# Kernel optimization log

Hardware: AMD Instinct MI355X
Metric: run time of the kernel (lower is better)

## Reference

```python
import jax, jax.numpy as jnp
import numpy as np

HID, NH, NKV, HD, BASE = 1536, 24, 6, 64, 10000.0
G = NH // NKV  # kv groups


def setup_inputs() -> dict:
    key = jax.random.key(0)
    k1, k2, k3, k4, k5 = jax.random.split(key, 5)
    B, S = 2, 2048
    s = 0.02
    return {
        "hidden_states": jax.random.normal(k1, (B, S, HID), jnp.float32),
        "position_ids": jnp.broadcast_to(jnp.arange(S, dtype=jnp.int64)[None, :], (B, S)),
        "Wq": jax.random.normal(k2, (NH * HD, HID), jnp.float32) * s,
        "Wk": jax.random.normal(k3, (NKV * HD, HID), jnp.float32) * s,
        "Wv": jax.random.normal(k4, (NKV * HD, HID), jnp.float32) * s,
        "Wo": jax.random.normal(k5, (HID, NH * HD), jnp.float32) * s,
    }


def _rope_tables(seq_len, dtype):
    inv_freq = 1.0 / (BASE ** (jnp.arange(0, HD, 2, dtype=jnp.float32) / HD))
    t = jnp.arange(seq_len, dtype=jnp.float32)
    freqs = jnp.einsum("i,j->ij", t, inv_freq)          # [S, HD/2]
    emb = jnp.concatenate([freqs, freqs], axis=-1)       # [S, HD]
    return jnp.cos(emb).astype(dtype), jnp.sin(emb).astype(dtype)


def _rotate_half(x):
    x1, x2 = x[..., : HD // 2], x[..., HD // 2:]
    return jnp.concatenate([-x2, x1], axis=-1)


def reference(hidden_states, position_ids, Wq, Wk, Wv, Wo):
    B, S, _ = hidden_states.shape
    q = (hidden_states @ Wq.T).reshape(B, S, NH, HD).transpose(0, 2, 1, 3)   # [B,NH,S,D]
    k = (hidden_states @ Wk.T).reshape(B, S, NKV, HD).transpose(0, 2, 1, 3)  # [B,NKV,S,D]
    v = (hidden_states @ Wv.T).reshape(B, S, NKV, HD).transpose(0, 2, 1, 3)

    cos_t, sin_t = _rope_tables(S, hidden_states.dtype)
    cos = cos_t[position_ids][:, None]  # [B,1,S,D]
    sin = sin_t[position_ids][:, None]
    q = q * cos + _rotate_half(q) * sin
    k = k * cos + _rotate_half(k) * sin

    # GQA attention without materializing repeated K/V: view q as [B,NKV,G,S,D]
    qg = q.reshape(B, NKV, G, S, HD)
    scale = 1.0 / np.sqrt(HD)
    scores = jnp.einsum("bkgsd,bktd->bkgst", qg, k) * scale  # [B,NKV,G,S,S]
    causal = jnp.tril(jnp.ones((S, S), dtype=bool))
    scores = jnp.where(causal, scores, jnp.finfo(scores.dtype).min)
    probs = jax.nn.softmax(scores, axis=-1)
    out = jnp.einsum("bkgst,bktd->bkgsd", probs, v)          # [B,NKV,G,S,D]
    out = out.reshape(B, NH, S, HD).transpose(0, 2, 1, 3).reshape(B, S, NH * HD)
    return out @ Wo.T
```

## Files before the change

### kernel.cpp

```cpp
#include <hip/hip_runtime.h>
#include <hip/hip_bf16.h>

#define HIDN 1536
#define NH   24
#define NKV  6
#define HD   64
#define BB   2
#define SS   2048
#define MTOT (BB*SS)
#define NQKV 2304
#define NCHUNK 80
#define LOG2E 1.4426950408889634f

typedef __bf16 bf16x8 __attribute__((ext_vector_type(8)));
typedef float  f32x4  __attribute__((ext_vector_type(4)));
typedef unsigned short u16x8 __attribute__((ext_vector_type(8)));
typedef unsigned int   u32x2 __attribute__((ext_vector_type(2)));

typedef __attribute__((address_space(1))) const unsigned short as1_ushort;
typedef __attribute__((address_space(3))) unsigned short as3_ushort;

__device__ inline float bf2f(unsigned short u) {
    unsigned v = (unsigned)u << 16; float f; __builtin_memcpy(&f, &v, 4); return f;
}
__device__ inline unsigned short f2bf(float f) {
    unsigned u; __builtin_memcpy(&u, &f, 4);
    u = (u + 0x7FFFu + ((u >> 16) & 1u)) >> 16;
    return (unsigned short)u;
}
__device__ inline unsigned cvt_pk_bf16(float lo, float hi) {
    unsigned r;
    asm("v_cvt_pk_bf16_f32 %0, %1, %2" : "=v"(r) : "v"(lo), "v"(hi));
    return r;
}
__device__ inline float exp2_hw(float x) {
    float r;
    asm("v_exp_f32 %0, %1" : "=v"(r) : "v"(x));
    return r;
}
__device__ inline float rowmax16_dpp(float x) {
    int v, r;
    v = __float_as_int(x);
    r = __builtin_amdgcn_update_dpp(v, v, 0x121, 0xF, 0xF, false);
    x = fmaxf(x, __int_as_float(r));
    v = __float_as_int(x);
    r = __builtin_amdgcn_update_dpp(v, v, 0x122, 0xF, 0xF, false);
    x = fmaxf(x, __int_as_float(r));
    v = __float_as_int(x);
    r = __builtin_amdgcn_update_dpp(v, v, 0x124, 0xF, 0xF, false);
    x = fmaxf(x, __int_as_float(r));
    v = __float_as_int(x);
    r = __builtin_amdgcn_update_dpp(v, v, 0x128, 0xF, 0xF, false);
    x = fmaxf(x, __int_as_float(r));
    return x;
}

__global__ __launch_bounds__(256) void k_prep(const float* __restrict__ h_f,
                                              const float* __restrict__ Wq,
                                              const float* __restrict__ Wk,
                                              const float* __restrict__ Wv,
                                              const float* __restrict__ Wo,
                                              unsigned short* __restrict__ h_bf,
                                              unsigned short* __restrict__ qkv_w,
                                              unsigned short* __restrict__ Wo_bf,
                                              float2* __restrict__ cs) {
    int i = blockIdx.x * 256 + threadIdx.x;
    const int nH = MTOT * HIDN / 4;
    const int nQ = HIDN * HIDN / 4;
    const int nK = NKV * HD * HIDN / 4;
    const int nW = 2 * nQ + 2 * nK;
    if (i < nH + nW) {
        const float* src; unsigned short* dst; int j;
        if (i < nH)                    { src = h_f; dst = h_bf;                        j = i; }
        else if ((i -= nH) < nQ)       { src = Wq;  dst = qkv_w;                       j = i; }
        else if (i < nQ + nK)          { src = Wk;  dst = qkv_w + (size_t)nQ * 4;      j = i - nQ; }
        else if (i < nQ + 2 * nK)      { src = Wv;  dst = qkv_w + (size_t)(nQ + nK) * 4; j = i - nQ - nK; }
        else                           { src = Wo;  dst = Wo_bf;                       j = i - nQ - 2 * nK; }
        float4 v = reinterpret_cast<const float4*>(src)[j];
        ushort4 o;
        o.x = f2bf(v.x); o.y = f2bf(v.y); o.z = f2bf(v.z); o.w = f2bf(v.w);
        reinterpret_cast<ushort4*>(dst)[j] = o;
        return;
    }
    int k = i - (nH + nW);
    if (k < SS * 32) {
        int s = k >> 5, f = k & 31;
        double inv = pow(10000.0, -(double)f / 32.0);
        double ang = (double)s * inv;
        cs[k] = make_float2((float)cos(ang), (float)sin(ang));
    }
}

template <typename OutT>
__global__ __launch_bounds__(256) void gemm_bt(const unsigned short* __restrict__ A,
                                               const unsigned short* __restrict__ Bt,
                                               OutT* __restrict__ C,
                                               int N, int K) {
    __shared__ unsigned short Alds[2][128 * 64];
    __shared__ unsigned short Blds[2][128 * 64];
    int t = threadIdx.x;
    int lane = t & 63, w = t >> 6;
    int m0 = blockIdx.y * 128, n0 = blockIdx.x * 128;
    int wm = (w >> 1) * 64, wn = (w & 1) * 64;
    int cidx = lane & 15, quad = lane >> 4;
    int srow = lane >> 3, scol = (lane & 7) * 8;

    int srcoff[4], dstoff[4];
#pragma unroll
    for (int c = 0; c < 4; ++c) {
        int chunk = w + c * 4;
        int row = chunk * 8 + srow;
        int col = scol ^ ((row & 7) * 8);
        srcoff[c] = row * K + col;
        dstoff[c] = chunk * 512;
    }

    f32x4 zero = {0.f, 0.f, 0.f, 0.f};
    f32x4 acc[4][4];
#pragma unroll
    for (int mi = 0; mi < 4; ++mi)
#pragma unroll
        for (int ni = 0; ni < 4; ++ni) acc[mi][ni] = zero;

    const unsigned short* Ab = A + (size_t)m0 * K;
    const unsigned short* Bb = Bt + (size_t)n0 * K;

#pragma unroll
    for (int c = 0; c < 4; ++c) {
        __builtin_amdgcn_global_load_lds((as1_ushort*)(Ab + srcoff[c]),
                                         (as3_ushort*)&Alds[0][dstoff[c]], 16, 0, 0);
        __builtin_amdgcn_global_load_lds((as1_ushort*)(Bb + srcoff[c]),
                                         (as3_ushort*)&Blds[0][dstoff[c]], 16, 0, 0);
    }
    asm volatile("s_waitcnt vmcnt(0)" ::: "memory");
    __syncthreads();

    int nk = K >> 6;
    for (int kt = 0; kt < nk; ++kt) {
        int cur = kt & 1;
        if (kt + 1 < nk) {
            int koff = (kt + 1) * 64;
#pragma unroll
            for (int c = 0; c < 4; ++c) {
                __builtin_amdgcn_global_load_lds((as1_ushort*)(Ab + srcoff[c] + koff),
                                                 (as3_ushort*)&Alds[cur ^ 1][dstoff[c]], 16, 0, 0);
                __builtin_amdgcn_global_load_lds((as1_ushort*)(Bb + srcoff[c] + koff),
                                                 (as3_ushort*)&Blds[cur ^ 1][dstoff[c]], 16, 0, 0);
            }
        }
#pragma unroll
        for (int ka = 0; ka < 2; ++ka) {
            bf16x8 af[4], bfr[4];
#pragma unroll
            for (int mi = 0; mi < 4; ++mi) {
                int arow = wm + mi * 16 + cidx;
                af[mi] = *reinterpret_cast<bf16x8*>(
                    &Alds[cur][arow * 64 + ((ka * 32 + quad * 8) ^ ((arow & 7) * 8))]);
            }
#pragma unroll
            for (int ni = 0; ni < 4; ++ni) {
                int brow = wn + ni * 16 + cidx;
                bfr[ni] = *reinterpret_cast<bf16x8*>(
                    &Blds[cur][brow * 64 + ((ka * 32 + quad * 8) ^ ((brow & 7) * 8))]);
            }
#pragma unroll
            for (int mi = 0; mi < 4; ++mi)
#pragma unroll
                for (int ni = 0; ni < 4; ++ni)
                    acc[mi][ni] = __builtin_amdgcn_mfma_f32_16x16x32_bf16(af[mi], bfr[ni],
                                                                          acc[mi][ni], 0, 0, 0);
        }
        asm volatile("s_waitcnt vmcnt(0)" ::: "memory");
        __syncthreads();
    }
#pragma unroll
    for (int mi = 0; mi < 4; ++mi)
#pragma unroll
        for (int ni = 0; ni < 4; ++ni)
#pragma unroll
            for (int i = 0; i < 4; ++i) {
                int row = m0 + wm + mi * 16 + quad * 4 + i;
                int col = n0 + wn + ni * 16 + cidx;
                C[(size_t)row * N + col] = acc[mi][ni][i];
            }
}

__global__ __launch_bounds__(256) void gemm_qkv(const unsigned short* __restrict__ A,
                                                const unsigned short* __restrict__ Bt,
                                                const int* __restrict__ pos_ids,
                                                const float2* __restrict__ cs,
                                                unsigned short* __restrict__ q_p,
                                                unsigned short* __restrict__ k_p,
                                                unsigned short* __restrict__ v_p) {
    __shared__ unsigned short Alds[2][128 * 64];
    __shared__ unsigned short Blds[2][128 * 64];
    int t = threadIdx.x;
    int lane = t & 63, w = t >> 6;
    int m0 = blockIdx.y * 128, n0 = blockIdx.x * 128;
    int wm = (w >> 1) * 64, wn = (w & 1) * 64;
    int cidx = lane & 15, quad = lane >> 4;
    int srow = lane >> 3, scol = (lane & 7) * 8;

    int srcoff[4], dstoff[4];
#pragma unroll
    for (int c = 0; c < 4; ++c) {
        int chunk = w + c * 4;
        int row = chunk * 8 + srow;
        int col = scol ^ ((row & 7) * 8);
        srcoff[c] = row * HIDN + col;
        dstoff[c] = chunk * 512;
    }

    f32x4 zero = {0.f, 0.f, 0.f, 0.f};
    f32x4 acc[4][4];
#pragma unroll
    for (int mi = 0; mi < 4; ++mi)
#pragma unroll
        for (int ni = 0; ni < 4; ++ni) acc[mi][ni] = zero;

    const unsigned short* Ab = A + (size_t)m0 * HIDN;
    const unsigned short* Bb = Bt + (size_t)n0 * HIDN;

#pragma unroll
    for (int c = 0; c < 4; ++c) {
        __builtin_amdgcn_global_load_lds((as1_ushort*)(Ab + srcoff[c]),
                                         (as3_ushort*)&Alds[0][dstoff[c]], 16, 0, 0);
        __builtin_amdgcn_global_load_lds((as1_ushort*)(Bb + srcoff[c]),
                                         (as3_ushort*)&Blds[0][dstoff[c]], 16, 0, 0);
    }
    asm volatile("s_waitcnt vmcnt(0)" ::: "memory");
    __syncthreads();

    const int nk = HIDN >> 6;
    for (int kt = 0; kt < nk; ++kt) {
        int cur = kt & 1;
        if (kt + 1 < nk) {
            int koff = (kt + 1) * 64;
#pragma unroll
            for (int c = 0; c < 4; ++c) {
                __builtin_amdgcn_global_load_lds((as1_ushort*)(Ab + srcoff[c] + koff),
                                                 (as3_ushort*)&Alds[cur ^ 1][dstoff[c]], 16, 0, 0);
                __builtin_amdgcn_global_load_lds((as1_ushort*)(Bb + srcoff[c] + koff),
                                                 (as3_ushort*)&Blds[cur ^ 1][dstoff[c]], 16, 0, 0);
            }
        }
#pragma unroll
        for (int ka = 0; ka < 2; ++ka) {
            bf16x8 af[4], bfr[4];
#pragma unroll
            for (int mi = 0; mi < 4; ++mi) {
                int arow = wm + mi * 16 + cidx;
                af[mi] = *reinterpret_cast<bf16x8*>(
                    &Alds[cur][arow * 64 + ((ka * 32 + quad * 8) ^ ((arow & 7) * 8))]);
            }
#pragma unroll
            for (int ni = 0; ni < 4; ++ni) {
                int brow = wn + ni * 16 + cidx;
                bfr[ni] = *reinterpret_cast<bf16x8*>(
                    &Blds[cur][brow * 64 + ((ka * 32 + quad * 8) ^ ((brow & 7) * 8))]);
            }
#pragma unroll
            for (int mi = 0; mi < 4; ++mi)
#pragma unroll
                for (int ni = 0; ni < 4; ++ni)
                    acc[mi][ni] = __builtin_amdgcn_mfma_f32_16x16x32_bf16(af[mi], bfr[ni],
                                                                          acc[mi][ni], 0, 0, 0);
        }
        asm volatile("s_waitcnt vmcnt(0)" ::: "memory");
        __syncthreads();
    }

    int colbase = n0 + wn;
    if (colbase >= NH * HD + NKV * HD) {
        int h = (colbase - (NH * HD + NKV * HD)) >> 6;
#pragma unroll
        for (int mi = 0; mi < 4; ++mi)
#pragma unroll
            for (int i = 0; i < 4; ++i) {
                int row = m0 + wm + mi * 16 + quad * 4 + i;
                int b = row >> 11, s = row & 2047;
                size_t base = ((size_t)(b * NKV + h) * SS + s) * 64;
#pragma unroll
                for (int ni = 0; ni < 4; ++ni)
                    v_p[base + ni * 16 + cidx] = f2bf(acc[mi][ni][i]);
            }
    } else {
        bool isQ = colbase < NH * HD;
        unsigned short* dst = isQ ? q_p : k_p;
        int h = isQ ? (colbase >> 6) : ((colbase - NH * HD) >> 6);
        int H = isQ ? NH : NKV;
        float scl = isQ ? (0.125f * LOG2E) : 1.0f;
#pragma unroll
        for (int mi = 0; mi < 4; ++mi)
#pragma unroll
            for (int i = 0; i < 4; ++i) {
                int row = m0 + wm + mi * 16 + quad * 4 + i;
                int b = row >> 11, s = row & 2047;
                int pos = pos_ids[row];
                float2 c1 = cs[pos * 32 + cidx];
                float2 c2 = cs[pos * 32 + 16 + cidx];
                size_t base = ((size_t)(b * H + h) * SS + s) * 64;
                float x10 = acc[mi][0][i], x20 = acc[mi][2][i];
                float x11 = acc[mi][1][i], x21 = acc[mi][3][i];
                dst[base + cidx]       = f2bf((x10 * c1.x - x20 * c1.y) * scl);
                dst[base + 32 + cidx]  = f2bf((x20 * c1.x + x10 * c1.y) * scl);
                dst[base + 16 + cidx]  = f2bf((x11 * c2.x - x21 * c2.y) * scl);
                dst[base + 48 + cidx]  = f2bf((x21 * c2.x + x11 * c2.y) * scl);
            }
    }
}

#define TRR(dst, ADDR, OFF) asm volatile("ds_read_b64_tr_b16 %0, %1 offset:" #OFF \
                                         : "=v"(dst) : "v"(ADDR))

__global__ __launch_bounds__(256, 4) void k_attn(const unsigned short* __restrict__ Qp,
                                                 const unsigned short* __restrict__ Kp,
                                                 const unsigned short* __restrict__ Vp,
                                                 unsigned short* __restrict__ part_acc,
                                                 float* __restrict__ part_ml,
                                                 unsigned short* __restrict__ a_out) {
    int bxr = NCHUNK - 1 - (int)blockIdx.x;
    int h = blockIdx.y, b = blockIdx.z;
    int kvh = h >> 2;
    int qt = 0, c = 0, g;
    {
        g = (bxr >= 48) ? 3 : (bxr >= 24) ? 2 : (bxr >= 8) ? 1 : 0;
        int b0 = 4 * g * (g + 1);
        int idx = bxr - b0;
        qt = 8 * g + idx / (g + 1);
        c = idx % (g + 1);
    }
    int p = (b * NH + h) * NCHUNK + bxr;
    int qbase = qt * 64, ck0 = c * 512;
    int nt = min(8, qt + 1 - c * 8);

    int t = threadIdx.x, lane = t & 63, w = t >> 6;
    int cidx = lane & 15, quad = lane >> 4;
    int qrow0 = qbase + w * 16;

    const unsigned short* qptr  = Qp + ((size_t)(b * NH + h) * SS + qrow0) * HD;
    const unsigned short* kbase = Kp + (((size_t)(b * NKV + kvh) * SS) + ck0) * HD;
    const unsigned short* vbase = Vp + (((size_t)(b * NKV + kvh) * SS) + ck0) * HD;

    __shared__ unsigned short Klds[2 * 4096];
    __shared__ unsigned short Vt[2 * 4096];
    __shared__ unsigned short Pt[4][64 * 16];

    const unsigned short* ksrc[2];
    const unsigned short* vsrc[2];
#pragma unroll
    for (int i = 0; i < 2; ++i) {
        int o = (w * 2 + i) * 512 + lane * 8;
        int kh = o >> 10, ka_ = (o >> 9) & 1, kq = (o >> 7) & 3, kc = (o >> 3) & 15;
        ksrc[i] = kbase + (kh * 16 + kc) * HD + ka_ * 32 + kq * 8;
        int r = o & 1023;
        int kv = ((r >> 6) << 2) | ((r >> 4) & 3);
        int d  = ((o >> 10) << 4) | (r & 15);
        vsrc[i] = vbase + kv * HD + d;
    }

    bf16x8 qa[2];
#pragma unroll
    for (int ka = 0; ka < 2; ++ka)
        qa[ka] = *reinterpret_cast<const bf16x8*>(qptr + (size_t)cidx * HD + ka * 32 + quad * 8);

    bf16x8 ones;
    {
        unsigned short ob = 0x3F80;
        u16x8 ov;
#pragma unroll
        for (int j = 0; j < 8; ++j) ov[j] = ob;
        __builtin_memcpy(&ones, &ov, 16);
    }

    f32x4 zero = {0.f, 0.f, 0.f, 0.f};
    f32x4 acc[4], acc_l = zero;
    float m_run[4];
#pragma unroll
    for (int i = 0; i < 4; ++i) { acc[i] = zero; m_run[i] = -1e30f; }

#pragma unroll
    for (int i = 0; i < 2; ++i) {
        __builtin_amdgcn_global_load_lds((as1_ushort*)ksrc[i],
                                         (as3_ushort*)&Klds[(w * 2 + i) * 512], 16, 0, 0);
        __builtin_amdgcn_global_load_lds((as1_ushort*)vsrc[i],
                                         (as3_ushort*)&Vt[(w * 2 + i) * 512], 16, 0, 0);
    }
    asm volatile("s_waitcnt vmcnt(0)" ::: "memory");
    __syncthreads();

    unsigned vtb  = (unsigned)(uintptr_t)(as3_ushort*)&Vt[0];
    unsigned va_base = vtb + (unsigned)(quad * 256 + cidx * 8);
    unsigned ptb  = (unsigned)(uintptr_t)(as3_ushort*)&Pt[w][0];
    unsigned va_p = ptb + (unsigned)(quad * 256 + cidx * 8);
    char* pwr = (char*)&Pt[w][0] + cidx * 32 + quad * 8;

    for (int it = 0; it < nt; ++it) {
        int cur = it & 1;
        int kvb = ck0 + it * 64;

        if (it + 1 < nt) {
            size_t nv = (size_t)(it + 1) * 64 * HD;
#pragma unroll
            for (int i = 0; i < 2; ++i) {
                __builtin_amdgcn_global_load_lds(
                    (as1_ushort*)(ksrc[i] + nv),
                    (as3_ushort*)&Klds[(cur ^ 1) * 4096 + (w * 2 + i) * 512], 16, 0, 0);
                __builtin_amdgcn_global_load_lds(
                    (as1_ushort*)(vsrc[i] + nv),
                    (as3_ushort*)&Vt[(cur ^ 1) * 4096 + (w * 2 + i) * 512], 16, 0, 0);
            }
        }

        bf16x8 kb[4][2];
#pragma unroll
        for (int ht = 0; ht < 4; ++ht)
#pragma unroll
            for (int ka = 0; ka < 2; ++ka)
                kb[ht][ka] = *reinterpret_cast<bf16x8*>(
                    &Klds[cur * 4096 + ht * 1024 + ka * 512 + quad * 128 + cidx * 8]);
        f32x4 sc[4];
#pragma unroll
        for (int ht = 0; ht < 4; ++ht) {
            f32x4 cacc = zero;
            cacc = __builtin_amdgcn_mfma_f32_16x16x32_bf16(qa[0], kb[ht][0], cacc, 0, 0, 0);
            cacc = __builtin_amdgcn_mfma_f32_16x16x32_bf16(qa[1], kb[ht][1], cacc, 0, 0, 0);
            sc[ht] = cacc;
        }

        unsigned va = va_base + (unsigned)(cur * 8192);
        u32x2 tv[4][4];
        TRR(tv[0][0], va, 0);    TRR(tv[0][1], va, 128);
        TRR(tv[0][2], va, 1024); TRR(tv[0][3], va, 1152);
        TRR(tv[1][0], va, 2048); TRR(tv[1][1], va, 2176);
        TRR(tv[1][2], va, 3072); TRR(tv[1][3], va, 3200);
        TRR(tv[2][0], va, 4096); TRR(tv[2][1], va, 4224);
        TRR(tv[2][2], va, 5120); TRR(tv[2][3], va, 5248);
        TRR(tv[3][0], va, 6144); TRR(tv[3][1], va, 6272);
        TRR(tv[3][2], va, 7168); TRR(tv[3][3], va, 7296);

        if (kvb + 63 > qrow0) {
#pragma unroll
            for (int ht = 0; ht < 4; ++ht)
#pragma unroll
                for (int i = 0; i < 4; ++i)
                    if (kvb + ht * 16 + cidx > qrow0 + quad * 4 + i) sc[ht][i] = -1e30f;
        }

        float mx[4];
#pragma unroll
        for (int i = 0; i < 4; ++i) {
            mx[i] = fmaxf(fmaxf(sc[0][i], sc[1][i]), fmaxf(sc[2][i], sc[3][i]));
            mx[i] = rowmax16_dpp(mx[i]);
        }

        bool need = false;
#pragma unroll
        for (int i = 0; i < 4; ++i) need |= (mx[i] > m_run[i] + 11.5f);
        if (__any(need)) {
#pragma unroll
            for (int i = 0; i < 4; ++i) {
                float mnew = fmaxf(m_run[i], mx[i]);
                float scl = exp2_hw(m_run[i] - mnew);
                m_run[i] = mnew;
#pragma unroll
                for (int dt = 0; dt < 4; ++dt) acc[dt][i] *= scl;
                acc_l[i] *= scl;
            }
        }
#pragma unroll
        for (int i = 0; i < 4; ++i)
#pragma unroll
            for (int ht = 0; ht < 4; ++ht) sc[ht][i] = exp2_hw(sc[ht][i] - m_run[i]);

#pragma unroll
        for (int ht = 0; ht < 4; ++ht) {
            u32x2 pk;
            pk[0] = cvt_pk_bf16(sc[ht][0], sc[ht][1]);
            pk[1] = cvt_pk_bf16(sc[ht][2], sc[ht][3]);
            *reinterpret_cast<u32x2*>(pwr + ht * 512) = pk;
        }
        asm volatile("" ::: "memory");
        u32x2 pt_[4];
        TRR(pt_[0], va_p, 0);    TRR(pt_[1], va_p, 128);
        TRR(pt_[2], va_p, 1024); TRR(pt_[3], va_p, 1152);
        asm volatile("s_waitcnt lgkmcnt(0)" ::: "memory");
        __builtin_amdgcn_sched_barrier(0);

        union { u32x2 a[2]; bf16x8 v; } up0, up1;
        up0.a[0] = pt_[0]; up0.a[1] = pt_[1];
        up1.a[0] = pt_[2]; up1.a[1] = pt_[3];
        bf16x8 pa0 = up0.v, pa1 = up1.v;

        __builtin_amdgcn_s_setprio(1);
        acc_l = __builtin_amdgcn_mfma_f32_16x16x32_bf16(pa0, ones, acc_l, 0, 0, 0);
        acc_l = __builtin_amdgcn_mfma_f32_16x16x32_bf16(pa1, ones, acc_l, 0, 0, 0);
#pragma unroll
        for (int dt = 0; dt < 4; ++dt) {
            union { u32x2 a[2]; bf16x8 v; } u0, u1;
            u0.a[0] = tv[dt][0]; u0.a[1] = tv[dt][1];
            u1.a[0] = tv[dt][2]; u1.a[1] = tv[dt][3];
            acc[dt] = __builtin_amdgcn_mfma_f32_16x16x32_bf16(pa0, u0.v, acc[dt], 0, 0, 0);
            acc[dt] = __builtin_amdgcn_mfma_f32_16x16x32_bf16(pa1, u1.v, acc[dt], 0, 0, 0);
        }
        __builtin_amdgcn_s_setprio(0);

        asm volatile("s_waitcnt vmcnt(0)" ::: "memory");
        __syncthreads();
    }

    if (g == 0) {
        float rl[4];
#pragma unroll
        for (int i = 0; i < 4; ++i) rl[i] = 1.f / acc_l[i];
#pragma unroll
        for (int dt = 0; dt < 4; ++dt)
#pragma unroll
            for (int i = 0; i < 4; ++i) {
                int row = qrow0 + quad * 4 + i;
                size_t o = ((size_t)(b * SS) + row) * HIDN + h * HD + dt * 16 + cidx;
                a_out[o] = f2bf(acc[dt][i] * rl[i]);
            }
    } else {
#pragma unroll
        for (int dt = 0; dt < 4; ++dt)
#pragma unroll
            for (int i = 0; i < 4; ++i) {
                int row = w * 16 + quad * 4 + i;
                part_acc[((size_t)p * 64 + row) * 64 + dt * 16 + cidx] = f2bf(acc[dt][i]);
            }
        if (cidx == 0) {
#pragma unroll
            for (int i = 0; i < 4; ++i) {
                int row = w * 16 + quad * 4 + i;
                part_ml[((size_t)p * 64 + row) * 2 + 0] = m_run[i];
                part_ml[((size_t)p * 64 + row) * 2 + 1] = acc_l[i];
            }
        }
    }
}

__global__ __launch_bounds__(256) void k_combine(const unsigned short* __restrict__ part_acc,
                                                 const float* __restrict__ part_ml,
                                                 unsigned short* __restrict__ a_out) {
    int idx = blockIdx.x * 256 + threadIdx.x;
    int d = idx & 63;
    int tmp = idx >> 6;
    int h = tmp % NH;
    int m2 = tmp / NH;
    int b = m2 / (SS - 512);
    int s = 512 + m2 % (SS - 512);
    int qt = s >> 6, row = s & 63;
    int g = qt >> 3;
    int off = 4 * g * (g + 1) + (qt & 7) * (g + 1);
    int C = g + 1;
    int pb = (b * NH + h) * NCHUNK + off;

    float2 ml[4];
    float M = -1e30f;
#pragma unroll
    for (int cc = 0; cc < 4; ++cc) {
        if (cc < C) {
            ml[cc] = *reinterpret_cast<const float2*>(&part_ml[((size_t)(pb + cc) * 64 + row) * 2]);
            M = fmaxf(M, ml[cc].x);
        } else {
            ml[cc] = make_float2(-1e30f, 0.f);
        }
    }
    float L = 0.f, O = 0.f;
#pragma unroll
    for (int cc = 0; cc < 4; ++cc) {
        if (cc < C) {
            float wgt = exp2_hw(ml[cc].x - M);
            L += ml[cc].y * wgt;
            O += bf2f(part_acc[((size_t)(pb + cc) * 64 + row) * 64 + d]) * wgt;
        }
    }
    a_out[((size_t)(b * SS) + s) * HIDN + h * 64 + d] = f2bf(O / L);
}

extern "C" void kernel_launch(void* const* d_in, const int* in_sizes, int n_in,
                              void* d_out, int out_size, void* d_ws, size_t ws_size,
                              hipStream_t stream) {
    (void)in_sizes; (void)n_in; (void)out_size; (void)ws_size;
    const float* h_f  = (const float*)d_in[0];
    const int*   pos  = (const int*)d_in[1];
    const float* Wq_f = (const float*)d_in[2];
    const float* Wk_f = (const float*)d_in[3];
    const float* Wv_f = (const float*)d_in[4];
    const float* Wo_f = (const float*)d_in[5];
    float* out = (float*)d_out;

    char* ws = (char*)d_ws;
    size_t off = 0;
    auto alloc = [&](size_t bytes) -> void* {
        void* p = ws + off;
        off += (bytes + 255) & ~(size_t)255;
        return p;
    };
    unsigned short* region0 = (unsigned short*)alloc((size_t)48 * NCHUNK * 64 * 64 * 2);
    unsigned short* h_bf     = region0;
    unsigned short* part_acc = region0;
    unsigned short* qkv_w  = (unsigned short*)alloc((size_t)NQKV * HIDN * 2);
    unsigned short* Wo_bf  = (unsigned short*)alloc((size_t)HIDN * NH * HD * 2);
    unsigned short* q_p    = (unsigned short*)alloc((size_t)MTOT * NH * HD * 2);
    unsigned short* k_p    = (unsigned short*)alloc((size_t)MTOT * NKV * HD * 2);
    unsigned short* v_p    = (unsigned short*)alloc((size_t)MTOT * NKV * HD * 2);
    unsigned short* a_out  = (unsigned short*)alloc((size_t)MTOT * HIDN * 2);
    float2* cs = (float2*)alloc((size_t)SS * 32 * 8);
    float* part_ml = (float*)alloc((size_t)BB * NH * NCHUNK * 64 * 2 * 4);

    {
        int nH = MTOT * HIDN / 4;
        int nW = 2 * (HIDN * HIDN / 4) + 2 * (NKV * HD * HIDN / 4);
        int total = nH + nW + SS * 32;
        k_prep<<<total / 256, 256, 0, stream>>>(h_f, Wq_f, Wk_f, Wv_f, Wo_f,
                                                h_bf, qkv_w, Wo_bf, cs);
    }

    gemm_qkv<<<dim3(NQKV / 128, MTOT / 128), 256, 0, stream>>>(
        h_bf, qkv_w, pos, cs, q_p, k_p, v_p);

    k_attn<<<dim3(NCHUNK, NH, BB), 256, 0, stream>>>(q_p, k_p, v_p, part_acc, part_ml, a_out);
    k_combine<<<(MTOT * NH * HD * 3 / 4) / 256, 256, 0, stream>>>(part_acc, part_ml, a_out);

    gemm_bt<float><<<dim3(HIDN / 128, MTOT / 128), 256, 0, stream>>>(
        a_out, Wo_bf, out, HIDN, HIDN);
}
```

Baseline: 205.0 us.

## Transpose score MFMA so each lane owns one query row in attention

The attention kernel now swaps the MFMA operands (K·Q instead of Q·K), so each lane holds scores for a single query row across 16 keys. That turns the per-row max and sum into scalar per-lane values reduced with two cross-quad shuffles, replacing the DPP row reductions and the ones-vector MFMA that computed the row sum. P is stored to a padded LDS layout and read back with plain 128-bit loads instead of transposing reads, and V·P uses swapped operands. Outputs are written as packed 4-element bf16 stores. The risk is more shuffle traffic and possible LDS bank conflicts in the new P layout.

Result: slower. 212.5 us (+3.7%).

```diff
diff --git a/kernel.cpp b/kernel.cpp
--- a/kernel.cpp
+++ b/kernel.cpp
@@ -37,22 +37,6 @@
     float r;
     asm("v_exp_f32 %0, %1" : "=v"(r) : "v"(x));
     return r;
-}
-__device__ inline float rowmax16_dpp(float x) {
-    int v, r;
-    v = __float_as_int(x);
-    r = __builtin_amdgcn_update_dpp(v, v, 0x121, 0xF, 0xF, false);
-    x = fmaxf(x, __int_as_float(r));
-    v = __float_as_int(x);
-    r = __builtin_amdgcn_update_dpp(v, v, 0x122, 0xF, 0xF, false);
-    x = fmaxf(x, __int_as_float(r));
-    v = __float_as_int(x);
-    r = __builtin_amdgcn_update_dpp(v, v, 0x124, 0xF, 0xF, false);
-    x = fmaxf(x, __int_as_float(r));
-    v = __float_as_int(x);
-    r = __builtin_amdgcn_update_dpp(v, v, 0x128, 0xF, 0xF, false);
-    x = fmaxf(x, __int_as_float(r));
-    return x;
 }
 
 __global__ __launch_bounds__(256) void k_prep(const float* __restrict__ h_f,
@@ -337,6 +321,7 @@
     int t = threadIdx.x, lane = t & 63, w = t >> 6;
     int cidx = lane & 15, quad = lane >> 4;
     int qrow0 = qbase + w * 16;
+    int myq = qrow0 + cidx;
 
     const unsigned short* qptr  = Qp + ((size_t)(b * NH + h) * SS + qrow0) * HD;
     const unsigned short* kbase = Kp + (((size_t)(b * NKV + kvh) * SS) + ck0) * HD;
@@ -344,7 +329,7 @@
 
     __shared__ unsigned short Klds[2 * 4096];
     __shared__ unsigned short Vt[2 * 4096];
-    __shared__ unsigned short Pt[4][64 * 16];
+    __shared__ unsigned short Pt[4][16 * 72];
 
     const unsigned short* ksrc[2];
     const unsigned short* vsrc[2];
@@ -364,20 +349,11 @@
     for (int ka = 0; ka < 2; ++ka)
         qa[ka] = *reinterpret_cast<const bf16x8*>(qptr + (size_t)cidx * HD + ka * 32 + quad * 8);
 
-    bf16x8 ones;
-    {
-        unsigned short ob = 0x3F80;
-        u16x8 ov;
-#pragma unroll
-        for (int j = 0; j < 8; ++j) ov[j] = ob;
-        __builtin_memcpy(&ones, &ov, 16);
-    }
-
     f32x4 zero = {0.f, 0.f, 0.f, 0.f};
-    f32x4 acc[4], acc_l = zero;
-    float m_run[4];
-#pragma unroll
-    for (int i = 0; i < 4; ++i) { acc[i] = zero; m_run[i] = -1e30f; }
+    f32x4 acc[4];
+    float acc_l = 0.f, m_run = -1e30f;
+#pragma unroll
+    for (int i = 0; i < 4; ++i) acc[i] = zero;
 
 #pragma unroll
     for (int i = 0; i < 2; ++i) {
@@ -391,9 +367,9 @@
 
     unsigned vtb  = (unsigned)(uintptr_t)(as3_ushort*)&Vt[0];
     unsigned va_base = vtb + (unsigned)(quad * 256 + cidx * 8);
-    unsigned ptb  = (unsigned)(uintptr_t)(as3_ushort*)&Pt[w][0];
-    unsigned va_p = ptb + (unsigned)(quad * 256 + cidx * 8);
-    char* pwr = (char*)&Pt[w][0] + cidx * 32 + quad * 8;
+    char* pbase = (char*)&Pt[w][0];
+    char* pwr = pbase + cidx * 144 + quad * 8;
+    char* prd = pbase + cidx * 144 + quad * 16;
 
     for (int it = 0; it < nt; ++it) {
         int cur = it & 1;
@@ -423,8 +399,8 @@
 #pragma unroll
         for (int ht = 0; ht < 4; ++ht) {
             f32x4 cacc = zero;
-            cacc = __builtin_amdgcn_mfma_f32_16x16x32_bf16(qa[0], kb[ht][0], cacc, 0, 0, 0);
-            cacc = __builtin_amdgcn_mfma_f32_16x16x32_bf16(qa[1], kb[ht][1], cacc, 0, 0, 0);
+            cacc = __builtin_amdgcn_mfma_f32_16x16x32_bf16(kb[ht][0], qa[0], cacc, 0, 0, 0);
+            cacc = __builtin_amdgcn_mfma_f32_16x16x32_bf16(kb[ht][1], qa[1], cacc, 0, 0, 0);
             sc[ht] = cacc;
         }
 
@@ -444,64 +420,63 @@
             for (int ht = 0; ht < 4; ++ht)
 #pragma unroll
                 for (int i = 0; i < 4; ++i)
-                    if (kvb + ht * 16 + cidx > qrow0 + quad * 4 + i) sc[ht][i] = -1e30f;
-        }
-
-        float mx[4];
-#pragma unroll
-        for (int i = 0; i < 4; ++i) {
-            mx[i] = fmaxf(fmaxf(sc[0][i], sc[1][i]), fmaxf(sc[2][i], sc[3][i]));
-            mx[i] = rowmax16_dpp(mx[i]);
-        }
-
-        bool need = false;
-#pragma unroll
-        for (int i = 0; i < 4; ++i) need |= (mx[i] > m_run[i] + 11.5f);
-        if (__any(need)) {
-#pragma unroll
-            for (int i = 0; i < 4; ++i) {
-                float mnew = fmaxf(m_run[i], mx[i]);
-                float scl = exp2_hw(m_run[i] - mnew);
-                m_run[i] = mnew;
-#pragma unroll
-                for (int dt = 0; dt < 4; ++dt) acc[dt][i] *= scl;
-                acc_l[i] *= scl;
-            }
-        }
-#pragma unroll
-        for (int i = 0; i < 4; ++i)
-#pragma unroll
-            for (int ht = 0; ht < 4; ++ht) sc[ht][i] = exp2_hw(sc[ht][i] - m_run[i]);
+                    if (kvb + ht * 16 + quad * 4 + i > myq) sc[ht][i] = -1e30f;
+        }
+
+        f32x4 m4 = sc[0];
+#pragma unroll
+        for (int i = 0; i < 4; ++i) m4[i] = fmaxf(fmaxf(sc[0][i], sc[1][i]),
+                                                  fmaxf(sc[2][i], sc[3][i]));
+        float mx = fmaxf(fmaxf(m4[0], m4[1]), fmaxf(m4[2], m4[3]));
+        mx = fmaxf(mx, __shfl_xor(mx, 16, 64));
+        mx = fmaxf(mx, __shfl_xor(mx, 32, 64));
+
+        if (__any(mx > m_run + 11.5f)) {
+            float mnew = fmaxf(m_run, mx);
+            float scl = exp2_hw(m_run - mnew);
+            m_run = mnew;
+#pragma unroll
+            for (int dt = 0; dt < 4; ++dt)
+#pragma unroll
+                for (int i = 0; i < 4; ++i) acc[dt][i] *= scl;
+            acc_l *= scl;
+        }
+#pragma unroll
+        for (int ht = 0; ht < 4; ++ht)
+#pragma unroll
+            for (int i = 0; i < 4; ++i) sc[ht][i] = exp2_hw(sc[ht][i] - m_run);
+
+        {
+            f32x4 s4;
+#pragma unroll
+            for (int i = 0; i < 4; ++i) s4[i] = (sc[0][i] + sc[1][i]) + (sc[2][i] + sc[3][i]);
+            float rs = (s4[0] + s4[1]) + (s4[2] + s4[3]);
+            rs += __shfl_xor(rs, 16, 64);
+            rs += __shfl_xor(rs, 32, 64);
+            acc_l += rs;
+        }
 
 #pragma unroll
         for (int ht = 0; ht < 4; ++ht) {
             u32x2 pk;
             pk[0] = cvt_pk_bf16(sc[ht][0], sc[ht][1]);
             pk[1] = cvt_pk_bf16(sc[ht][2], sc[ht][3]);
-            *reinterpret_cast<u32x2*>(pwr + ht * 512) = pk;
+            *reinterpret_cast<u32x2*>(pwr + ht * 32) = pk;
         }
         asm volatile("" ::: "memory");
-        u32x2 pt_[4];
-        TRR(pt_[0], va_p, 0);    TRR(pt_[1], va_p, 128);
-        TRR(pt_[2], va_p, 1024); TRR(pt_[3], va_p, 1152);
+        bf16x8 pb0 = *reinterpret_cast<bf16x8*>(prd);
+        bf16x8 pb1 = *reinterpret_cast<bf16x8*>(prd + 64);
         asm volatile("s_waitcnt lgkmcnt(0)" ::: "memory");
         __builtin_amdgcn_sched_barrier(0);
 
-        union { u32x2 a[2]; bf16x8 v; } up0, up1;
-        up0.a[0] = pt_[0]; up0.a[1] = pt_[1];
-        up1.a[0] = pt_[2]; up1.a[1] = pt_[3];
-        bf16x8 pa0 = up0.v, pa1 = up1.v;
-
         __builtin_amdgcn_s_setprio(1);
-        acc_l = __builtin_amdgcn_mfma_f32_16x16x32_bf16(pa0, ones, acc_l, 0, 0, 0);
-        acc_l = __builtin_amdgcn_mfma_f32_16x16x32_bf16(pa1, ones, acc_l, 0, 0, 0);
 #pragma unroll
         for (int dt = 0; dt < 4; ++dt) {
             union { u32x2 a[2]; bf16x8 v; } u0, u1;
             u0.a[0] = tv[dt][0]; u0.a[1] = tv[dt][1];
             u1.a[0] = tv[dt][2]; u1.a[1] = tv[dt][3];
-            acc[dt] = __builtin_amdgcn_mfma_f32_16x16x32_bf16(pa0, u0.v, acc[dt], 0, 0, 0);
-            acc[dt] = __builtin_amdgcn_mfma_f32_16x16x32_bf16(pa1, u1.v, acc[dt], 0, 0, 0);
+            acc[dt] = __builtin_amdgcn_mfma_f32_16x16x32_bf16(u0.v, pb0, acc[dt], 0, 0, 0);
+            acc[dt] = __builtin_amdgcn_mfma_f32_16x16x32_bf16(u1.v, pb1, acc[dt], 0, 0, 0);
         }
         __builtin_amdgcn_s_setprio(0);
 
@@ -510,32 +485,28 @@
     }
 
     if (g == 0) {
-        float rl[4];
-#pragma unroll
-        for (int i = 0; i < 4; ++i) rl[i] = 1.f / acc_l[i];
-#pragma unroll
-        for (int dt = 0; dt < 4; ++dt)
-#pragma unroll
-            for (int i = 0; i < 4; ++i) {
-                int row = qrow0 + quad * 4 + i;
-                size_t o = ((size_t)(b * SS) + row) * HIDN + h * HD + dt * 16 + cidx;
-                a_out[o] = f2bf(acc[dt][i] * rl[i]);
-            }
+        float rl = 1.f / acc_l;
+        size_t rowbase = ((size_t)(b * SS) + myq) * HIDN + h * HD + quad * 4;
+#pragma unroll
+        for (int dt = 0; dt < 4; ++dt) {
+            u32x2 o;
+            o[0] = cvt_pk_bf16(acc[dt][0] * rl, acc[dt][1] * rl);
+            o[1] = cvt_pk_bf16(acc[dt][2] * rl, acc[dt][3] * rl);
+            *reinterpret_cast<u32x2*>(&a_out[rowbase + dt * 16]) = o;
+        }
     } else {
-#pragma unroll
-        for (int dt = 0; dt < 4; ++dt)
-#pragma unroll
-            for (int i = 0; i < 4; ++i) {
-                int row = w * 16 + quad * 4 + i;
-                part_acc[((size_t)p * 64 + row) * 64 + dt * 16 + cidx] = f2bf(acc[dt][i]);
-            }
-        if (cidx == 0) {
-#pragma unroll
-            for (int i = 0; i < 4; ++i) {
-                int row = w * 16 + quad * 4 + i;
-                part_ml[((size_t)p * 64 + row) * 2 + 0] = m_run[i];
-                part_ml[((size_t)p * 64 + row) * 2 + 1] = acc_l[i];
-            }
+        size_t rowbase = ((size_t)p * 64 + w * 16 + cidx) * 64 + quad * 4;
+#pragma unroll
+        for (int dt = 0; dt < 4; ++dt) {
+            u32x2 o;
+            o[0] = cvt_pk_bf16(acc[dt][0], acc[dt][1]);
+            o[1] = cvt_pk_bf16(acc[dt][2], acc[dt][3]);
+            *reinterpret_cast<u32x2*>(&part_acc[rowbase + dt * 16]) = o;
+        }
+        if (lane < 16) {
+            size_t mlb = ((size_t)p * 64 + w * 16 + cidx) * 2;
+            part_ml[mlb + 0] = m_run;
+            part_ml[mlb + 1] = acc_l;
         }
     }
 }
```
